# Performance work log

Measured on AMD Instinct MI355X. Metric: run time of the kernel, lower is better.

Reference implementation:

```python
import jax, jax.numpy as jnp
import numpy as np

N, T, D = 20000, 60, 20      # nodes, window length, input features
H = 128                      # lstm_hidden
G = 128                      # gnn_hidden
HEADS = 4
C = G // HEADS               # per-head channels (gnn_hidden // heads)
E = 320000                   # directed edges
OUT = 2
NEG_SLOPE = 0.2              # PyG GATConv leaky-relu slope


def setup_inputs() -> dict:
    key = jax.random.key(0)
    ks = jax.random.split(key, 16)
    s = lambda k, shape, sc=0.05: jax.random.normal(k, shape, jnp.float32) * sc
    return {
        "x_win": jax.random.normal(ks[0], (N, T, D), jnp.float32),
        "edge_index": jax.random.randint(ks[1], (2, E), 0, N),
        # LSTM (1 layer, PyTorch gate order i,f,g,o)
        "Wih": s(ks[2], (4 * H, D)),
        "Whh": s(ks[3], (4 * H, H)),
        "bih": s(ks[4], (4 * H,)),
        "bhh": s(ks[5], (4 * H,)),
        # GAT layer 1
        "W1": s(ks[6], (H, G)),
        "att_src1": s(ks[7], (HEADS, C)),
        "att_dst1": s(ks[8], (HEADS, C)),
        "b1": s(ks[9], (G,)),
        # GAT layer 2
        "W2": s(ks[10], (G, G)),
        "att_src2": s(ks[11], (HEADS, C)),
        "att_dst2": s(ks[12], (HEADS, C)),
        "b2": s(ks[13], (G,)),
        # linear head
        "Wh": s(ks[14], (G, OUT)),
        "bh": s(ks[15], (OUT,)),
    }


def _lstm_last(x, Wih, Whh, bih, bhh):
    """Single-layer LSTM over [N, T, D]; return last hidden state [N, H]."""
    n = x.shape[0]
    h0 = jnp.zeros((n, Whh.shape[1]), x.dtype)
    c0 = jnp.zeros_like(h0)
    b = bih + bhh

    def step(carry, xt):
        h, c = carry
        gates = xt @ Wih.T + h @ Whh.T + b
        i, f, g, o = jnp.split(gates, 4, axis=-1)
        c = jax.nn.sigmoid(f) * c + jax.nn.sigmoid(i) * jnp.tanh(g)
        h = jax.nn.sigmoid(o) * jnp.tanh(c)
        return (h, c), None

    (h, _), _ = jax.lax.scan(step, (h0, c0), jnp.swapaxes(x, 0, 1))
    return h


def _gat(x, src, dst, W, a_src, a_dst, bias):
    """PyG-style GATConv (self-loops already in src/dst), concat heads + bias."""
    n = x.shape[0]
    xh = (x @ W).reshape(n, HEADS, C)                 # [N, heads, C]
    asr = (xh * a_src[None]).sum(-1)                  # [N, heads]
    adt = (xh * a_dst[None]).sum(-1)                  # [N, heads]
    e = jax.nn.leaky_relu(asr[src] + adt[dst], NEG_SLOPE)   # [E+N, heads]
    # per-destination softmax (numerically stable segment softmax)
    emax = jax.ops.segment_max(e, dst, num_segments=n)
    ex = jnp.exp(e - emax[dst])
    denom = jax.ops.segment_sum(ex, dst, num_segments=n)
    alpha = ex / (denom[dst] + 1e-16)                 # [E+N, heads]
    out = jax.ops.segment_sum(alpha[:, :, None] * xh[src], dst, num_segments=n)
    return out.reshape(n, HEADS * C) + bias


def reference(x_win, edge_index, Wih, Whh, bih, bhh,
              W1, att_src1, att_dst1, b1,
              W2, att_src2, att_dst2, b2, Wh, bh):
    node = _lstm_last(x_win, Wih, Whh, bih, bhh)      # dropout = identity (eval)
    loops = jnp.arange(N, dtype=edge_index.dtype)
    src = jnp.concatenate([edge_index[0], loops])     # add self-loops (PyG default)
    dst = jnp.concatenate([edge_index[1], loops])
    h = jax.nn.elu(_gat(node, src, dst, W1, att_src1, att_dst1, b1))
    h = jax.nn.elu(_gat(h, src, dst, W2, att_src2, att_dst2, b2))
    return h @ Wh + bh                                # [N, 2]
```

## Files before the change

kernel.cpp:

```cpp
#include <hip/hip_runtime.h>
#include <hip/hip_bf16.h>

#define NN 20000
#define TT 60
#define DD 20
#define HH 128
#define KK 148
#define EE 320000
#define EA 340000
#define ZSTRIDE 168
#define MROWS 80

typedef unsigned short u16;
typedef unsigned int u32;
typedef __attribute__((ext_vector_type(8))) short bf16x8;
typedef __attribute__((ext_vector_type(4))) float f32x4;

#define LOG2E  1.44269504088896340f
#define LOG2E2 2.88539008177792681f

__device__ __forceinline__ float bf2f(u16 u){ return __uint_as_float(((u32)u)<<16); }
__device__ __forceinline__ u16 f2bf(float f){
  u32 x = __float_as_uint(f);
  return (u16)((x + 0x7FFFu + ((x >> 16) & 1u)) >> 16);
}
__device__ __forceinline__ float sig2(float x){
  return __builtin_amdgcn_rcpf(1.f + __builtin_amdgcn_exp2f(-x));
}
__device__ __forceinline__ float tanh2(float x){
  return fmaf(-2.f, __builtin_amdgcn_rcpf(1.f + __builtin_amdgcn_exp2f(x)), 1.f);
}
__device__ __forceinline__ float sigf(float x){
  return __builtin_amdgcn_rcpf(1.f + __expf(-x));
}

__global__ void prep_lstm_kernel(const float* __restrict__ Wih, const float* __restrict__ Whh,
                                 const float* __restrict__ bih, const float* __restrict__ bhh,
                                 u16* __restrict__ Wfrag){
  int idx = blockIdx.x*256 + threadIdx.x;
  if (idx >= 8*4*5*64*8) return;
  int j    = idx & 7;
  int lane = (idx >> 3) & 63;
  int rest = idx >> 9;
  int kt = rest % 5, q = (rest/5) & 3, w = rest/20;
  int col = q*128 + w*16 + (lane & 15);
  int k   = kt*32 + ((lane >> 4) & 3)*8 + j;
  float v = 0.f;
  if (k < DD)       v = Wih[(size_t)col*DD + k];
  else if (k < KK)  v = Whh[(size_t)col*HH + (k - DD)];
  else if (k == KK) v = bih[col] + bhh[col];
  v *= (q == 2) ? LOG2E2 : LOG2E;
  Wfrag[idx] = f2bf(v);
}

__global__ void prep_w_kernel(const float* __restrict__ W1, const float* __restrict__ W2,
                              u16* __restrict__ W1f, u16* __restrict__ W2f){
  int idx = blockIdx.x*256 + threadIdx.x;
  const float* W = W1; u16* Wf = W1f;
  if (idx >= 8*4*64*8){ idx -= 8*4*64*8; W = W2; Wf = W2f; }
  int j = idx & 7, lane = (idx>>3) & 63, kt = (idx>>9) & 3, ct = idx>>11;
  int col = ct*16 + (lane & 15);
  int k   = kt*32 + ((lane>>4) & 3)*8 + j;
  Wf[idx] = f2bf(W[(size_t)k*128 + col]);
}

__global__ __launch_bounds__(512, 2) void lstm_kernel(const float* __restrict__ xwin,
    const u16* __restrict__ Wfrag, u16* __restrict__ node_h){
  __shared__ u16 z[2][MROWS][ZSTRIDE];
  const int tid  = threadIdx.x;
  const int lane = tid & 63;
  const int w    = tid >> 6;
  const int nb   = blockIdx.x * MROWS;
  const int l15  = lane & 15;
  const int quad = lane >> 4;

  bf16x8 B[4][5];
  {
    const bf16x8* bp = (const bf16x8*)Wfrag;
    #pragma unroll
    for (int q = 0; q < 4; q++)
      #pragma unroll
      for (int kt = 0; kt < 5; kt++)
        B[q][kt] = bp[(size_t)((w*20 + q*5 + kt)*64 + lane)];
  }

  for (int i = tid; i < 2*MROWS*(ZSTRIDE/2); i += 512) ((u32*)(&z[0][0][0]))[i] = 0;

  const float* xp[4]; int nrow[4], ecol[4], vld[4];
  #pragma unroll
  for (int k2 = 0; k2 < 4; k2++){
    int s = tid + k2*512;
    vld[k2] = (s < MROWS*DD);
    int ss = vld[k2] ? s : 0;
    nrow[k2] = ss/DD; ecol[k2] = ss - nrow[k2]*DD;
    xp[k2] = xwin + (size_t)(nb + nrow[k2])*(TT*DD) + ecol[k2];
  }

  __syncthreads();
  #pragma unroll
  for (int k2 = 0; k2 < 4; k2++)
    if (vld[k2]) z[0][nrow[k2]][ecol[k2]] = f2bf(xp[k2][0]);
  if (tid < 2*MROWS){
    int b = tid >= MROWS, r = tid - b*MROWS;
    z[b][r][KK] = 0x3F80;
  }

  f32x4 cst[5];
  const f32x4 zf = {0.f, 0.f, 0.f, 0.f};
  #pragma unroll
  for (int mt = 0; mt < 5; mt++) cst[mt] = zf;
  __syncthreads();

  #pragma unroll 1
  for (int t = 0; t < TT; t++){
    const int cur = t & 1, nxt = cur ^ 1;
    const int pre = (t + 1 < TT);

    float xf[4];
    #pragma unroll
    for (int k2 = 0; k2 < 4; k2++)
      xf[k2] = (pre && vld[k2]) ? xp[k2][(t+1)*DD] : 0.f;

    #pragma unroll
    for (int mt = 0; mt < 5; mt++){
      bf16x8 A[5];
      #pragma unroll
      for (int kt = 0; kt < 5; kt++)
        A[kt] = *(const bf16x8*)&z[cur][mt*16 + l15][kt*32 + quad*8];

      f32x4 acc[4];
      #pragma unroll
      for (int q = 0; q < 4; q++){
        f32x4 a = __builtin_amdgcn_mfma_f32_16x16x32_bf16(A[0], B[q][0], zf, 0,0,0);
        a = __builtin_amdgcn_mfma_f32_16x16x32_bf16(A[1], B[q][1], a, 0,0,0);
        a = __builtin_amdgcn_mfma_f32_16x16x32_bf16(A[2], B[q][2], a, 0,0,0);
        a = __builtin_amdgcn_mfma_f32_16x16x32_bf16(A[3], B[q][3], a, 0,0,0);
        a = __builtin_amdgcn_mfma_f32_16x16x32_bf16(A[4], B[q][4], a, 0,0,0);
        acc[q] = a;
      }

      f32x4 cv = cst[mt];
      #pragma unroll
      for (int r = 0; r < 4; r++){
        float si = sig2(acc[0][r]);
        float sf = sig2(acc[1][r]);
        float tg = tanh2(acc[2][r]);
        float so = sig2(acc[3][r]);
        float cc = fmaf(sf, cv[r], si*tg);
        cv[r] = cc;
        float h = so * tanh2(cc * LOG2E2);
        const int row = mt*16 + quad*4 + r;
        u16 hb = f2bf(h);
        z[nxt][row][DD + w*16 + l15] = hb;
        if (t == TT-1)
          node_h[(size_t)(nb + row)*HH + w*16 + l15] = hb;
      }
      cst[mt] = cv;
    }

    if (pre){
      #pragma unroll
      for (int k2 = 0; k2 < 4; k2++)
        if (vld[k2]) z[nxt][nrow[k2]][ecol[k2]] = f2bf(xf[k2]);
    }
    __syncthreads();
  }
}

__global__ __launch_bounds__(256) void gemm_kernel(const u16* __restrict__ X,
    const u16* __restrict__ Wf, u16* __restrict__ Y){
  __shared__ u16 xs[32][136];
  const int tid = threadIdx.x, lane = tid & 63, w = tid >> 6;
  const int l15 = lane & 15, quad = lane >> 4;
  const int rb  = blockIdx.x*32;

  for (int c = tid; c < 512; c += 256){
    int row = c >> 4, cc = c & 15;
    *(bf16x8*)&xs[row][cc*8] = *(const bf16x8*)&X[(size_t)(rb+row)*128 + cc*8];
  }
  bf16x8 Bf[2][4];
  #pragma unroll
  for (int ct = 0; ct < 2; ct++)
    #pragma unroll
    for (int kt = 0; kt < 4; kt++)
      Bf[ct][kt] = *(const bf16x8*)&Wf[(size_t)((((2*w+ct)*4 + kt)*64 + lane))*8];
  __syncthreads();

  bf16x8 A[2][4];
  #pragma unroll
  for (int mt = 0; mt < 2; mt++)
    #pragma unroll
    for (int kt = 0; kt < 4; kt++)
      A[mt][kt] = *(const bf16x8*)&xs[mt*16 + l15][kt*32 + quad*8];

  const f32x4 zf = {0.f,0.f,0.f,0.f};
  #pragma unroll
  for (int mt = 0; mt < 2; mt++)
    #pragma unroll
    for (int ct = 0; ct < 2; ct++){
      f32x4 a = __builtin_amdgcn_mfma_f32_16x16x32_bf16(A[mt][0], Bf[ct][0], zf, 0,0,0);
      a = __builtin_amdgcn_mfma_f32_16x16x32_bf16(A[mt][1], Bf[ct][1], a, 0,0,0);
      a = __builtin_amdgcn_mfma_f32_16x16x32_bf16(A[mt][2], Bf[ct][2], a, 0,0,0);
      a = __builtin_amdgcn_mfma_f32_16x16x32_bf16(A[mt][3], Bf[ct][3], a, 0,0,0);
      #pragma unroll
      for (int r = 0; r < 4; r++)
        Y[(size_t)(rb + mt*16 + quad*4 + r)*128 + (2*w+ct)*16 + l15] = f2bf(a[r]);
    }
}

__global__ __launch_bounds__(256) void att_kernel(const u16* __restrict__ XH,
    const float* __restrict__ att_s, const float* __restrict__ att_d,
    float* __restrict__ asr, float* __restrict__ adt){
  __shared__ float as_[128], ad_[128];
  int tid = threadIdx.x;
  if (tid < 128){ as_[tid] = att_s[tid]; ad_[tid] = att_d[tid]; }
  __syncthreads();
  int n = blockIdx.x*64 + (tid>>2);
  int h = tid & 3;
  if (n >= NN) return;
  const u16* row = XH + (size_t)n*128 + h*32;
  float sv = 0.f, dv = 0.f;
  #pragma unroll
  for (int blk = 0; blk < 4; blk++){
    bf16x8 v = *(const bf16x8*)(row + blk*8);
    #pragma unroll
    for (int j = 0; j < 8; j++){
      float x = bf2f((u16)v[j]);
      sv = fmaf(x, as_[h*32 + blk*8 + j], sv);
      dv = fmaf(x, ad_[h*32 + blk*8 + j], dv);
    }
  }
  asr[n*4+h] = sv; adt[n*4+h] = dv;
}

__device__ __forceinline__ void edge_sd(int e, const int* src, const int* dst, int& s, int& d){
  if (e < EE){ s = src[e]; d = dst[e]; } else { s = e - EE; d = s; }
}

__global__ void deg_kernel(const int* __restrict__ src, const int* __restrict__ dst,
                           int* __restrict__ deg){
  int e = blockIdx.x*256 + threadIdx.x;
  if (e >= EA) return;
  int s, d; edge_sd(e, src, dst, s, d);
  atomicAdd(deg + d, 1);
}

#define SCB 80
__global__ __launch_bounds__(256) void psum_kernel(const int* __restrict__ deg,
                                                   int* __restrict__ psum){
  __shared__ int ws[4];
  int i = blockIdx.x*256 + threadIdx.x;
  int v = (i < NN) ? deg[i] : 0;
  #pragma unroll
  for (int off = 32; off > 0; off >>= 1) v += __shfl_down(v, off);
  if ((threadIdx.x & 63) == 0) ws[threadIdx.x >> 6] = v;
  __syncthreads();
  if (threadIdx.x == 0) psum[blockIdx.x] = ws[0]+ws[1]+ws[2]+ws[3];
}

__global__ void pscan_kernel(const int* __restrict__ psum, int* __restrict__ boff,
                             int* __restrict__ rowptr){
  if (threadIdx.x == 0){
    int acc = 0;
    for (int b = 0; b < SCB; b++){ boff[b] = acc; acc += psum[b]; }
    boff[SCB] = acc;
    rowptr[NN] = acc;
  }
}

__global__ __launch_bounds__(256) void rowptr_kernel(const int* __restrict__ deg,
    const int* __restrict__ boff, int* __restrict__ rowptr, int* __restrict__ cursor){
  __shared__ int buf[256];
  const int tid = threadIdx.x;
  int i = blockIdx.x*256 + tid;
  int v = (i < NN) ? deg[i] : 0;
  buf[tid] = v;
  __syncthreads();
  #pragma unroll
  for (int off = 1; off < 256; off <<= 1){
    int t = (tid >= off) ? buf[tid - off] : 0;
    __syncthreads();
    buf[tid] += t;
    __syncthreads();
  }
  if (i < NN){
    int excl = buf[tid] - v + boff[blockIdx.x];
    rowptr[i] = excl; cursor[i] = excl;
  }
}

__global__ void fill_kernel(const int* __restrict__ src, const int* __restrict__ dst,
                            int* __restrict__ cursor, int* __restrict__ elist){
  int e = blockIdx.x*256 + threadIdx.x;
  if (e >= EA) return;
  int s, d; edge_sd(e, src, dst, s, d);
  int pos = atomicAdd(cursor + d, 1);
  elist[pos] = s;
}

__global__ __launch_bounds__(512) void gat_kernel(const int* __restrict__ rowptr,
    const int* __restrict__ elist, const float* __restrict__ asr,
    const float* __restrict__ adt, const u16* __restrict__ XH,
    const float* __restrict__ bias, u16* __restrict__ out,
    const float* __restrict__ Wh, const float* __restrict__ bh,
    float* __restrict__ outf){
  const int tid = threadIdx.x, lane = tid & 63, w = tid >> 6;
  const int d = blockIdx.x*8 + w;
  const int r0 = rowptr[d], r1 = rowptr[d+1];
  const int h = lane >> 4;
  const int c = lane*2;
  float4 ad4 = *(const float4*)(adt + (size_t)d*4);
  const float adh = (h==0) ? ad4.x : (h==1) ? ad4.y : (h==2) ? ad4.z : ad4.w;

  float den = 0.f, accx = 0.f, accy = 0.f;
  int s_cur = elist[r0];
  float4 a_cur = *(const float4*)(asr + (size_t)s_cur*4);
  u32 pk_cur = ((const u32*)XH)[(size_t)s_cur*64 + lane];
  for (int idx = r0; idx < r1; idx++){
    int s_nxt = (idx+1 < r1) ? elist[idx+1] : s_cur;
    float4 a_nxt = *(const float4*)(asr + (size_t)s_nxt*4);
    u32 pk_nxt = ((const u32*)XH)[(size_t)s_nxt*64 + lane];
    float av = (h==0) ? a_cur.x : (h==1) ? a_cur.y : (h==2) ? a_cur.z : a_cur.w;
    float l = av + adh; l = l > 0.f ? l : 0.2f*l;
    float ex = __expf(l);
    den += ex;
    accx = fmaf(ex, bf2f((u16)pk_cur),       accx);
    accy = fmaf(ex, bf2f((u16)(pk_cur>>16)), accy);
    a_cur = a_nxt; pk_cur = pk_nxt; s_cur = s_nxt;
  }
  float rd = __builtin_amdgcn_rcpf(den);
  float vx = accx*rd + bias[c], vy = accy*rd + bias[c+1];
  vx = vx > 0.f ? vx : __expf(vx) - 1.f;
  vy = vy > 0.f ? vy : __expf(vy) - 1.f;

  if (Wh == nullptr){
    u32 pk = (u32)f2bf(vx) | ((u32)f2bf(vy) << 16);
    ((u32*)out)[(size_t)d*64 + lane] = pk;
  } else {
    float p0 = vx*Wh[c*2]   + vy*Wh[c*2+2];
    float p1 = vx*Wh[c*2+1] + vy*Wh[c*2+3];
    #pragma unroll
    for (int off = 32; off > 0; off >>= 1){
      p0 += __shfl_xor(p0, off);
      p1 += __shfl_xor(p1, off);
    }
    if (lane == 0){
      float2 o; o.x = p0 + bh[0]; o.y = p1 + bh[1];
      ((float2*)outf)[d] = o;
    }
  }
}

extern "C" void kernel_launch(void* const* d_in, const int* in_sizes, int n_in,
                              void* d_out, int out_size, void* d_ws, size_t ws_size,
                              hipStream_t stream){
  const float* xwin = (const float*)d_in[0];
  const int*   eidx = (const int*)d_in[1];
  const float* Wih  = (const float*)d_in[2];
  const float* Whh  = (const float*)d_in[3];
  const float* bih  = (const float*)d_in[4];
  const float* bhh  = (const float*)d_in[5];
  const float* W1   = (const float*)d_in[6];
  const float* as1  = (const float*)d_in[7];
  const float* ad1  = (const float*)d_in[8];
  const float* b1   = (const float*)d_in[9];
  const float* W2   = (const float*)d_in[10];
  const float* as2  = (const float*)d_in[11];
  const float* ad2  = (const float*)d_in[12];
  const float* b2   = (const float*)d_in[13];
  const float* Wh   = (const float*)d_in[14];
  const float* bh   = (const float*)d_in[15];
  const int* src = eidx;
  const int* dst = eidx + EE;

  char* ws = (char*)d_ws;
  size_t off = 0;
  auto alloc = [&](size_t bytes)->void*{
    void* p = ws + off; off += (bytes + 255) & ~(size_t)255; return p;
  };
  u16*   WfL   = (u16*)  alloc((size_t)8*4*5*64*8*sizeof(u16));
  u16*   W1f   = (u16*)  alloc((size_t)8*4*64*8*sizeof(u16));
  u16*   W2f   = (u16*)  alloc((size_t)8*4*64*8*sizeof(u16));
  u16*   nodeh = (u16*)  alloc((size_t)NN*128*sizeof(u16));
  u16*   xh    = (u16*)  alloc((size_t)NN*128*sizeof(u16));
  u16*   hbuf  = (u16*)  alloc((size_t)NN*128*sizeof(u16));
  float* asr   = (float*)alloc((size_t)NN*4*sizeof(float));
  float* adt   = (float*)alloc((size_t)NN*4*sizeof(float));
  int*   deg   = (int*)  alloc((size_t)NN*sizeof(int));
  int*   rowp  = (int*)  alloc((size_t)(NN+1)*sizeof(int));
  int*   curs  = (int*)  alloc((size_t)NN*sizeof(int));
  int*   psum  = (int*)  alloc((size_t)SCB*sizeof(int));
  int*   boff  = (int*)  alloc((size_t)(SCB+1)*sizeof(int));
  int*   elist = (int*)  alloc((size_t)EA*sizeof(int));
  (void)ws_size; (void)in_sizes; (void)n_in; (void)out_size;

  const int EGRID = (EA+255)/256;

  prep_lstm_kernel<<<(8*4*5*64*8+255)/256, 256, 0, stream>>>(Wih, Whh, bih, bhh, WfL);
  prep_w_kernel<<<(2*8*4*64*8+255)/256, 256, 0, stream>>>(W1, W2, W1f, W2f);
  hipMemsetAsync(deg, 0, (size_t)NN*sizeof(int), stream);
  deg_kernel<<<EGRID, 256, 0, stream>>>(src, dst, deg);
  psum_kernel<<<SCB, 256, 0, stream>>>(deg, psum);
  pscan_kernel<<<1, 64, 0, stream>>>(psum, boff, rowp);
  rowptr_kernel<<<SCB, 256, 0, stream>>>(deg, boff, rowp, curs);
  fill_kernel<<<EGRID, 256, 0, stream>>>(src, dst, curs, elist);

  lstm_kernel<<<NN/MROWS, 512, 0, stream>>>(xwin, WfL, nodeh);

  gemm_kernel<<<NN/32, 256, 0, stream>>>(nodeh, W1f, xh);
  att_kernel<<<(NN+63)/64, 256, 0, stream>>>(xh, as1, ad1, asr, adt);
  gat_kernel<<<NN/8, 512, 0, stream>>>(rowp, elist, asr, adt, xh, b1, hbuf,
                                       nullptr, nullptr, nullptr);
  gemm_kernel<<<NN/32, 256, 0, stream>>>(hbuf, W2f, xh);
  att_kernel<<<(NN+63)/64, 256, 0, stream>>>(xh, as2, ad2, asr, adt);
  gat_kernel<<<NN/8, 512, 0, stream>>>(rowp, elist, asr, adt, xh, b2, nullptr,
                                       Wh, bh, (float*)d_out);
}
```

Baseline: 531.0 us.

## Split LSTM row tiles across 16 waves per block and use hardware bf16 convert

```diff
diff --git a/kernel.cpp b/kernel.cpp
--- a/kernel.cpp
+++ b/kernel.cpp
@@ -24,14 +24,16 @@
   u32 x = __float_as_uint(f);
   return (u16)((x + 0x7FFFu + ((x >> 16) & 1u)) >> 16);
 }
+__device__ __forceinline__ u16 f2bf_cvt(float f){
+  float r;
+  asm("v_cvt_pk_bf16_f32 %0, %1, %2" : "=v"(r) : "v"(f), "v"(f));
+  return (u16)__float_as_uint(r);
+}
 __device__ __forceinline__ float sig2(float x){
   return __builtin_amdgcn_rcpf(1.f + __builtin_amdgcn_exp2f(-x));
 }
 __device__ __forceinline__ float tanh2(float x){
   return fmaf(-2.f, __builtin_amdgcn_rcpf(1.f + __builtin_amdgcn_exp2f(x)), 1.f);
-}
-__device__ __forceinline__ float sigf(float x){
-  return __builtin_amdgcn_rcpf(1.f + __expf(-x));
 }
 
 __global__ void prep_lstm_kernel(const float* __restrict__ Wih, const float* __restrict__ Whh,
@@ -42,8 +44,8 @@
   int j    = idx & 7;
   int lane = (idx >> 3) & 63;
   int rest = idx >> 9;
-  int kt = rest % 5, q = (rest/5) & 3, w = rest/20;
-  int col = q*128 + w*16 + (lane & 15);
+  int kt = rest % 5, q = (rest/5) & 3, wc = rest/20;
+  int col = q*128 + wc*16 + (lane & 15);
   int k   = kt*32 + ((lane >> 4) & 3)*8 + j;
   float v = 0.f;
   if (k < DD)       v = Wih[(size_t)col*DD + k];
@@ -64,12 +66,14 @@
   Wf[idx] = f2bf(W[(size_t)k*128 + col]);
 }
 
-__global__ __launch_bounds__(512, 2) void lstm_kernel(const float* __restrict__ xwin,
+__global__ __launch_bounds__(1024) void lstm_kernel(const float* __restrict__ xwin,
     const u16* __restrict__ Wfrag, u16* __restrict__ node_h){
   __shared__ u16 z[2][MROWS][ZSTRIDE];
   const int tid  = threadIdx.x;
   const int lane = tid & 63;
   const int w    = tid >> 6;
+  const int wc   = w & 7;
+  const int wm   = w >> 3;
   const int nb   = blockIdx.x * MROWS;
   const int l15  = lane & 15;
   const int quad = lane >> 4;
@@ -81,34 +85,28 @@
     for (int q = 0; q < 4; q++)
       #pragma unroll
       for (int kt = 0; kt < 5; kt++)
-        B[q][kt] = bp[(size_t)((w*20 + q*5 + kt)*64 + lane)];
-  }
-
-  for (int i = tid; i < 2*MROWS*(ZSTRIDE/2); i += 512) ((u32*)(&z[0][0][0]))[i] = 0;
-
-  const float* xp[4]; int nrow[4], ecol[4], vld[4];
-  #pragma unroll
-  for (int k2 = 0; k2 < 4; k2++){
-    int s = tid + k2*512;
-    vld[k2] = (s < MROWS*DD);
-    int ss = vld[k2] ? s : 0;
-    nrow[k2] = ss/DD; ecol[k2] = ss - nrow[k2]*DD;
-    xp[k2] = xwin + (size_t)(nb + nrow[k2])*(TT*DD) + ecol[k2];
-  }
-
-  __syncthreads();
-  #pragma unroll
-  for (int k2 = 0; k2 < 4; k2++)
-    if (vld[k2]) z[0][nrow[k2]][ecol[k2]] = f2bf(xp[k2][0]);
+        B[q][kt] = bp[(size_t)((wc*20 + q*5 + kt)*64 + lane)];
+  }
+
+  for (int i = tid; i < 2*MROWS*(ZSTRIDE/2); i += 1024) ((u32*)(&z[0][0][0]))[i] = 0;
+
+  const int n0 = tid/20,  e0 = tid - n0*20;
+  const int i1 = tid + 1024;
+  const int n1 = i1/20,   e1 = i1 - n1*20;
+  const int has1 = (i1 < MROWS*DD);
+  const float* p0 = xwin + (size_t)(nb + n0)*(TT*DD) + e0;
+  const float* p1 = xwin + (size_t)(nb + (has1 ? n1 : 0))*(TT*DD) + e1;
+
+  __syncthreads();
+  z[0][n0][e0] = f2bf_cvt(p0[0]);
+  if (has1) z[0][n1][e1] = f2bf_cvt(p1[0]);
   if (tid < 2*MROWS){
     int b = tid >= MROWS, r = tid - b*MROWS;
     z[b][r][KK] = 0x3F80;
   }
 
-  f32x4 cst[5];
   const f32x4 zf = {0.f, 0.f, 0.f, 0.f};
-  #pragma unroll
-  for (int mt = 0; mt < 5; mt++) cst[mt] = zf;
+  f32x4 c0 = zf, c1 = zf, c2 = zf;
   __syncthreads();
 
   #pragma unroll 1
@@ -116,13 +114,13 @@
     const int cur = t & 1, nxt = cur ^ 1;
     const int pre = (t + 1 < TT);
 
-    float xf[4];
-    #pragma unroll
-    for (int k2 = 0; k2 < 4; k2++)
-      xf[k2] = (pre && vld[k2]) ? xp[k2][(t+1)*DD] : 0.f;
-
-    #pragma unroll
-    for (int mt = 0; mt < 5; mt++){
+    float xf0 = 0.f, xf1 = 0.f;
+    if (pre){
+      xf0 = p0[(t+1)*DD];
+      if (has1) xf1 = p1[(t+1)*DD];
+    }
+
+    auto do_mt = [&](const int mt, f32x4& cv){
       bf16x8 A[5];
       #pragma unroll
       for (int kt = 0; kt < 5; kt++)
@@ -139,7 +137,6 @@
         acc[q] = a;
       }
 
-      f32x4 cv = cst[mt];
       #pragma unroll
       for (int r = 0; r < 4; r++){
         float si = sig2(acc[0][r]);
@@ -150,18 +147,22 @@
         cv[r] = cc;
         float h = so * tanh2(cc * LOG2E2);
         const int row = mt*16 + quad*4 + r;
-        u16 hb = f2bf(h);
-        z[nxt][row][DD + w*16 + l15] = hb;
+        u16 hb = f2bf_cvt(h);
+        z[nxt][row][DD + wc*16 + l15] = hb;
         if (t == TT-1)
-          node_h[(size_t)(nb + row)*HH + w*16 + l15] = hb;
+          node_h[(size_t)(nb + row)*HH + wc*16 + l15] = hb;
       }
-      cst[mt] = cv;
+    };
+
+    if (wm == 0){
+      do_mt(0, c0); do_mt(1, c1); do_mt(2, c2);
+    } else {
+      do_mt(3, c0); do_mt(4, c1);
     }
 
     if (pre){
-      #pragma unroll
-      for (int k2 = 0; k2 < 4; k2++)
-        if (vld[k2]) z[nxt][nrow[k2]][ecol[k2]] = f2bf(xf[k2]);
+      z[nxt][n0][e0] = f2bf_cvt(xf0);
+      if (has1) z[nxt][n1][e1] = f2bf_cvt(xf1);
     }
     __syncthreads();
   }
@@ -405,7 +406,7 @@
   rowptr_kernel<<<SCB, 256, 0, stream>>>(deg, boff, rowp, curs);
   fill_kernel<<<EGRID, 256, 0, stream>>>(src, dst, curs, elist);
 
-  lstm_kernel<<<NN/MROWS, 512, 0, stream>>>(xwin, WfL, nodeh);
+  lstm_kernel<<<NN/MROWS, 1024, 0, stream>>>(xwin, WfL, nodeh);
 
   gemm_kernel<<<NN/32, 256, 0, stream>>>(nodeh, W1f, xh);
   att_kernel<<<(NN+63)/64, 256, 0, stream>>>(xh, as1, ad1, asr, adt);
```

Result: slower. 630.5 us (+18.7%).
